# Kernel optimization log

Measured on AMD Instinct MI355X. Metric: run time of the kernel, lower is better.

## Reference

```python
import jax, jax.numpy as jnp
import numpy as np

DIM = 1024
HEADS = 16
DIM_HEAD = 64
DIM_INNER = HEADS * DIM_HEAD
SCALE = DIM_HEAD ** -0.5


def rmsnorm(x, w):
    eps = jnp.asarray(jnp.finfo(x.dtype).eps, x.dtype)
    var = jnp.mean(jnp.square(x), axis=-1, keepdims=True)
    return x * jax.lax.rsqrt(var + eps) * w


def setup_inputs() -> dict:
    key = jax.random.key(0)
    ks = jax.random.split(key, 6)
    tokens = jax.random.normal(ks[0], (2, 2048, DIM), dtype=jnp.float32)
    norm_w = jnp.ones((DIM,), dtype=jnp.float32)
    Wq = jax.random.normal(ks[1], (DIM, DIM_INNER), dtype=jnp.float32) * 0.02
    Wkv = jax.random.normal(ks[2], (DIM, 2 * DIM_INNER), dtype=jnp.float32) * 0.02
    Wout = jax.random.normal(ks[3], (DIM_INNER, DIM), dtype=jnp.float32) * 0.02
    Wg = jax.random.normal(ks[4], (DIM, HEADS), dtype=jnp.float32) * 0.02
    return {"tokens": tokens, "norm_w": norm_w, "Wq": Wq, "Wkv": Wkv, "Wout": Wout, "Wg": Wg}


def reference(tokens, norm_w, Wq, Wkv, Wout, Wg):
    b, n, _ = tokens.shape
    x = rmsnorm(tokens, norm_w)                      # [b, n, dim]
    q = x @ Wq                                       # [b, n, h*d]
    kv = x @ Wkv                                     # self-attention: context = tokens
    k, v = jnp.split(kv, 2, axis=-1)

    def split_heads(t):
        return t.reshape(b, n, HEADS, DIM_HEAD).transpose(0, 2, 1, 3)  # [b, h, n, d]

    q, k, v = map(split_heads, (q, k, v))

    sim = jnp.einsum('bhid,bhjd->bhij', q, k) * SCALE  # [b, h, n, n]
    causal_mask = jnp.triu(jnp.ones((n, n), dtype=bool), k=1)
    sim = jnp.where(causal_mask, jnp.asarray(-jnp.finfo(sim.dtype).max, sim.dtype), sim)
    attn = jax.nn.softmax(sim, axis=-1)
    out = jnp.einsum('bhij,bhjd->bhid', attn, v)       # [b, h, n, d]

    gates = jax.nn.sigmoid(x @ Wg)                     # [b, n, h]
    gates = gates.transpose(0, 2, 1)[..., None]        # [b, h, n, 1]
    out = gates * out

    out = out.transpose(0, 2, 1, 3).reshape(b, n, DIM_INNER)  # merge heads
    return out @ Wout                                  # [b, n, dim]
```

## Files before the change

### kernel.cpp

```cpp
#include <hip/hip_runtime.h>
#include <hip/hip_bf16.h>
#include <math.h>

constexpr int BB = 2;
constexpr int NN = 2048;
constexpr int DM = 1024;
constexpr int NH = 16;
constexpr int HD = 64;
constexpr int DI = NH * HD;
constexpr int MT = BB * NN;
constexpr float SM_SCALE = 0.125f * 1.44269504089f;

typedef __attribute__((ext_vector_type(8))) short short8v;
typedef __attribute__((ext_vector_type(4))) float f32x4;

__device__ inline unsigned cvt_pk_bf16(float lo, float hi) {
  unsigned r;
  asm("v_cvt_pk_bf16_f32 %0, %1, %2" : "=v"(r) : "v"(lo), "v"(hi));
  return r;
}
__device__ inline void pl32_swap(unsigned& a, unsigned& b) {
  asm("v_permlane32_swap_b32 %0, %1" : "+v"(a), "+v"(b));
}
__device__ inline void pl16_swap(unsigned& a, unsigned& b) {
  asm("v_permlane16_swap_b32 %0, %1" : "+v"(a), "+v"(b));
}
__device__ __forceinline__ void gload16(const void* g, void* l) {
  __builtin_amdgcn_global_load_lds(
      (const __attribute__((address_space(1))) unsigned int*)g,
      (__attribute__((address_space(3))) unsigned int*)l, 16, 0, 0);
}

__global__ __launch_bounds__(256) void k_prep(const float* __restrict__ tokens,
                                              const float* __restrict__ norm_w,
                                              const float* __restrict__ Wg,
                                              const float* __restrict__ Wq,
                                              const float* __restrict__ Wkv,
                                              const float* __restrict__ Wout,
                                              __hip_bfloat16* __restrict__ xb,
                                              float* __restrict__ g,
                                              __hip_bfloat16* __restrict__ Wqkvt,
                                              __hip_bfloat16* __restrict__ Woutt) {
  const int bid = blockIdx.x;
  const int t = threadIdx.x;
  if (bid < MT) {
    __shared__ float xs[DM];
    __shared__ float red[4];
    __shared__ float gred[4][16];
    const int tok = bid;
    float4 v = ((const float4*)(tokens + (size_t)tok * DM))[t];
    float ss = v.x * v.x + v.y * v.y + v.z * v.z + v.w * v.w;
#pragma unroll
    for (int m = 1; m < 64; m <<= 1) ss += __shfl_xor(ss, m, 64);
    if ((t & 63) == 0) red[t >> 6] = ss;
    __syncthreads();
    float tot = red[0] + red[1] + red[2] + red[3];
    float inv = rsqrtf(tot * (1.0f / DM) + 1.1920929e-7f);
    float4 wv = ((const float4*)norm_w)[t];
    float4 o;
    o.x = v.x * inv * wv.x;
    o.y = v.y * inv * wv.y;
    o.z = v.z * inv * wv.z;
    o.w = v.w * inv * wv.w;
    uint2 pk = make_uint2(cvt_pk_bf16(o.x, o.y), cvt_pk_bf16(o.z, o.w));
    *(uint2*)(xb + (size_t)tok * DM + t * 4) = pk;
    *(float4*)&xs[t * 4] = o;
    __syncthreads();
    const int h = t & 15, seg = t >> 4, wid = t >> 6;
    const float* xp = &xs[seg * 64];
    const float* wp = Wg + (size_t)(seg * 64) * NH + h;
    float s = 0.f;
#pragma unroll 8
    for (int k = 0; k < 64; k++) s = fmaf(xp[k], wp[(size_t)k * NH], s);
    s += __shfl_xor(s, 16);
    s += __shfl_xor(s, 32);
    if ((t & 63) < 16) gred[wid][h] = s;
    __syncthreads();
    if (t < 16) {
      float tot2 = gred[0][t] + gred[1][t] + gred[2][t] + gred[3][t];
      g[(size_t)tok * NH + t] = 1.f / (1.f + __expf(-tot2));
    }
  } else {
    const int wb = bid - MT;
    const int bx = wb & 127, by = wb >> 7;
    const int kb = by * 32;
    const float* W;
    __hip_bfloat16* dst;
    int N, col0, drow0;
    if (bx < 32) {
      W = Wq; N = DI; col0 = bx * 32; dst = Wqkvt; drow0 = col0;
    } else if (bx < 96) {
      W = Wkv; N = 2 * DI; col0 = (bx - 32) * 32; dst = Wqkvt; drow0 = DI + col0;
    } else {
      W = Wout; N = DM; col0 = (bx - 96) * 32; dst = Woutt; drow0 = col0;
    }
    __shared__ float tile[32][33];
    const int c = t & 31, r8 = t >> 5;
#pragma unroll
    for (int i = 0; i < 4; i++)
      tile[r8 + i * 8][c] = W[(size_t)(kb + r8 + i * 8) * N + col0 + c];
    __syncthreads();
#pragma unroll
    for (int i = 0; i < 4; i++)
      dst[(size_t)(drow0 + r8 + i * 8) * DM + kb + c] = __float2bfloat16(tile[c][r8 + i * 8]);
  }
}

template <int MODE, int BX>
__global__ __launch_bounds__(256) void k_mgemm(const __hip_bfloat16* __restrict__ A,
                                               const __hip_bfloat16* __restrict__ Bt,
                                               float* __restrict__ C,
                                               __hip_bfloat16* __restrict__ OQ,
                                               __hip_bfloat16* __restrict__ OK,
                                               __hip_bfloat16* __restrict__ OV, int Nc) {
  const int nwg = (int)gridDim.x;
  const int cpx = nwg >> 3;
  const int swz = (blockIdx.x & 7) * cpx + (blockIdx.x >> 3);
  const int bxi = swz % BX, byi = swz / BX;

  __shared__ __hip_bfloat16 As[128][32];
  __shared__ __hip_bfloat16 Bs[64][32];
  const int t = threadIdx.x, wid = t >> 6, lane = t & 63;
  const int lq = lane & 15, lg = lane >> 4;
  const int wr = wid >> 1, wc = wid & 1;
  const int m0 = byi * 128, n0 = bxi * 64;
  const int srow = lane >> 2, scol = (lane & 3) * 8;

  const __hip_bfloat16* Ag = A + (size_t)(m0 + wid * 32 + srow) * DM + scol;
  const __hip_bfloat16* Bg = Bt + (size_t)(n0 + wid * 16 + srow) * DM + scol;

  f32x4 acc[4][2];
#pragma unroll
  for (int i = 0; i < 4; i++)
#pragma unroll
    for (int j = 0; j < 2; j++) acc[i][j] = (f32x4){0.f, 0.f, 0.f, 0.f};

  for (int k0 = 0; k0 < DM; k0 += 32) {
    __syncthreads();
    gload16(Ag + k0, &As[wid * 32][0]);
    gload16(Ag + 16 * DM + k0, &As[wid * 32 + 16][0]);
    gload16(Bg + k0, &Bs[wid * 16][0]);
    __syncthreads();
    short8v af[4], bf[2];
#pragma unroll
    for (int i = 0; i < 4; i++) af[i] = *(const short8v*)&As[wr * 64 + i * 16 + lq][lg * 8];
#pragma unroll
    for (int j = 0; j < 2; j++) bf[j] = *(const short8v*)&Bs[wc * 32 + j * 16 + lq][lg * 8];
#pragma unroll
    for (int i = 0; i < 4; i++)
#pragma unroll
      for (int j = 0; j < 2; j++)
        acc[i][j] = __builtin_amdgcn_mfma_f32_16x16x32_bf16(af[i], bf[j], acc[i][j], 0, 0, 0);
  }

#pragma unroll
  for (int i = 0; i < 4; i++) {
    const int mb = m0 + wr * 64 + i * 16 + lg * 4;
#pragma unroll
    for (int j = 0; j < 2; j++) {
      const int c = n0 + wc * 32 + j * 16 + lq;
      if (MODE == 0) {
#pragma unroll
        for (int r = 0; r < 4; r++) C[(size_t)(mb + r) * Nc + c] = acc[i][j][r];
      } else {
        const int b = mb >> 11, nl = mb & (NN - 1);
        if (c < DI) {
          const int h = c >> 6, d = c & 63;
          __hip_bfloat16* dst = OQ + ((size_t)(b * NH + h) * NN + nl) * HD + d;
#pragma unroll
          for (int r = 0; r < 4; r++) dst[(size_t)r * HD] = __float2bfloat16(acc[i][j][r]);
        } else if (c < 2 * DI) {
          const int ck = c - DI;
          const int h = ck >> 6, d = ck & 63;
          __hip_bfloat16* dst = OK + ((size_t)(b * NH + h) * NN + nl) * HD + d;
#pragma unroll
          for (int r = 0; r < 4; r++) dst[(size_t)r * HD] = __float2bfloat16(acc[i][j][r]);
        } else {
          const int cd = c - 2 * DI;
          const int h = cd >> 6, d = cd & 63;
          uint2 pk = make_uint2(cvt_pk_bf16(acc[i][j][0], acc[i][j][1]),
                                cvt_pk_bf16(acc[i][j][2], acc[i][j][3]));
          *(uint2*)(OV + ((size_t)(b * NH + h) * HD + d) * NN + nl) = pk;
        }
      }
    }
  }
}

__global__ __launch_bounds__(64) void k_attn_mfma(const __hip_bfloat16* __restrict__ Qb,
                                                  const __hip_bfloat16* __restrict__ Kb,
                                                  const __hip_bfloat16* __restrict__ Vtb,
                                                  const float* __restrict__ gates,
                                                  __hip_bfloat16* __restrict__ aob,
                                                  float* __restrict__ Opart,
                                                  float* __restrict__ mpart,
                                                  float* __restrict__ lpart) {
  const int bid = blockIdx.x;
  const int xcd = bid & 7;
  const int s = bid >> 3;
  const int gq = s / 96;
  const int t = s % 96;
  const int bh = gq * 8 + xcd;
  const int i = t / 3, j = t % 3;
  int grp, kt0, kt1, chunk;
  if (j < 2) {
    grp = 63 - i;
    chunk = j;
    const int nt = (grp >> 1) + 1;
    const int h0 = (nt + 1) >> 1;
    kt0 = chunk ? h0 : 0;
    kt1 = chunk ? nt : h0;
  } else {
    grp = 31 - i;
    chunk = -1;
    kt0 = 0;
    kt1 = (grp >> 1) + 1;
  }
  const int lane = threadIdx.x;
  const int lg = lane >> 4, lq = lane & 15;
  const int q0 = grp * 32;

  const __hip_bfloat16* Qh = Qb + (size_t)bh * NN * HD;
  const __hip_bfloat16* Kh = Kb + (size_t)bh * NN * HD;
  const __hip_bfloat16* Vh = Vtb + (size_t)bh * HD * NN;

  short8v qf0[2], qf1[2];
#pragma unroll
  for (int ks = 0; ks < 2; ks++) {
    qf0[ks] = *(const short8v*)(Qh + (size_t)(q0 + lq) * HD + ks * 32 + lg * 8);
    qf1[ks] = *(const short8v*)(Qh + (size_t)(q0 + 16 + lq) * HD + ks * 32 + lg * 8);
  }

  f32x4 oacc0[4], oacc1[4];
#pragma unroll
  for (int jx = 0; jx < 4; jx++) {
    oacc0[jx] = (f32x4){0.f, 0.f, 0.f, 0.f};
    oacc1[jx] = (f32x4){0.f, 0.f, 0.f, 0.f};
  }
  float m0r = -3.0e38f, l0p = 0.f, m1r = -3.0e38f, l1p = 0.f;

  auto LOADK = [&](short8v (*kf)[2], int kt) {
    const int kvb = kt * 64;
#pragma unroll
    for (int jx = 0; jx < 4; jx++)
#pragma unroll
      for (int ks = 0; ks < 2; ks++)
        kf[jx][ks] = *(const short8v*)(Kh + (size_t)(kvb + jx * 16 + lq) * HD + ks * 32 + lg * 8);
  };
  auto LOADV = [&](short8v (*vf)[2], int kt) {
    const int kvb = kt * 64;
#pragma unroll
    for (int jx = 0; jx < 4; jx++)
#pragma unroll
      for (int ks = 0; ks < 2; ks++)
        vf[jx][ks] = *(const short8v*)(Vh + (size_t)(jx * 16 + lq) * NN + kvb + ks * 32 + lg * 8);
  };

  auto GROUP = [&](const short8v* qf, f32x4* oacc, float& m_run, float& l_part,
                   int q0g, const short8v (*kf)[2], const short8v (*vf)[2], int kt) {
    const int kvb = kt * 64;
    f32x4 sacc[4];
#pragma unroll
    for (int jx = 0; jx < 4; jx++) sacc[jx] = (f32x4){0.f, 0.f, 0.f, 0.f};
#pragma unroll
    for (int jx = 0; jx < 4; jx++)
#pragma unroll
      for (int ks = 0; ks < 2; ks++)
        sacc[jx] = __builtin_amdgcn_mfma_f32_16x16x32_bf16(kf[jx][ks], qf[ks], sacc[jx], 0, 0, 0);

    const int qg = q0g + lq;
    const bool diag = (kvb + 63 > q0g);
    float ss[4][4];
#pragma unroll
    for (int jx = 0; jx < 4; jx++)
#pragma unroll
      for (int r = 0; r < 4; r++) {
        float v = sacc[jx][r] * SM_SCALE;
        if (diag && (kvb + jx * 16 + lg * 4 + r > qg)) v = -3.0e38f;
        ss[jx][r] = v;
      }

    float tmax = -3.0e38f;
#pragma unroll
    for (int jx = 0; jx < 4; jx++)
#pragma unroll
      for (int r = 0; r < 4; r++) tmax = fmaxf(tmax, ss[jx][r]);

    if (!__all(tmax <= m_run + 8.0f)) {
      float tr = fmaxf(tmax, __shfl_xor(tmax, 16));
      tr = fmaxf(tr, __shfl_xor(tr, 32));
      const float mnew = fmaxf(m_run, tr);
      const float cf = exp2f(m_run - mnew);
      l_part *= cf;
#pragma unroll
      for (int jx = 0; jx < 4; jx++)
#pragma unroll
        for (int r = 0; r < 4; r++) oacc[jx][r] *= cf;
      m_run = mnew;
    }

    float psum = 0.f;
    unsigned upk[4], vpk[4];
#pragma unroll
    for (int jx = 0; jx < 4; jx++) {
      float p0 = exp2f(ss[jx][0] - m_run), p1 = exp2f(ss[jx][1] - m_run);
      float p2 = exp2f(ss[jx][2] - m_run), p3 = exp2f(ss[jx][3] - m_run);
      psum += (p0 + p1) + (p2 + p3);
      upk[jx] = cvt_pk_bf16(p0, p1);
      vpk[jx] = cvt_pk_bf16(p2, p3);
    }
    l_part += psum;

#pragma unroll
    for (int ks = 0; ks < 2; ks++) {
      unsigned w0 = upk[2 * ks], w2 = upk[2 * ks + 1];
      unsigned w1 = vpk[2 * ks], w3 = vpk[2 * ks + 1];
      pl32_swap(w0, w2);
      pl16_swap(w0, w2);
      pl32_swap(w1, w3);
      pl16_swap(w1, w3);
      int4 bw = make_int4((int)w0, (int)w1, (int)w2, (int)w3);
      short8v pb = __builtin_bit_cast(short8v, bw);
#pragma unroll
      for (int jx = 0; jx < 4; jx++)
        oacc[jx] = __builtin_amdgcn_mfma_f32_16x16x32_bf16(vf[jx][ks], pb, oacc[jx], 0, 0, 0);
    }
  };

  short8v kfA[4][2], kfB[4][2], vf[4][2];
  LOADK(kfA, kt0);
  int kt = kt0;
  while (true) {
    LOADV(vf, kt);
    if (kt + 1 < kt1) LOADK(kfB, kt + 1);
    GROUP(qf0, oacc0, m0r, l0p, q0, kfA, vf, kt);
    GROUP(qf1, oacc1, m1r, l1p, q0 + 16, kfA, vf, kt);
    if (++kt == kt1) break;
    LOADV(vf, kt);
    if (kt + 1 < kt1) LOADK(kfA, kt + 1);
    GROUP(qf0, oacc0, m0r, l0p, q0, kfB, vf, kt);
    GROUP(qf1, oacc1, m1r, l1p, q0 + 16, kfB, vf, kt);
    if (++kt == kt1) break;
  }

  float l0 = l0p + __shfl_xor(l0p, 16);
  l0 += __shfl_xor(l0, 32);
  float l1 = l1p + __shfl_xor(l1p, 16);
  l1 += __shfl_xor(l1, 32);

  if (chunk >= 0) {
    const int gi = grp - 32;
    const size_t pidx = (size_t)(bh * 32 + gi) * 2 + chunk;
    float* Op = Opart + pidx * 2048;
#pragma unroll
    for (int jx = 0; jx < 4; jx++) {
      *(f32x4*)(Op + lq * 64 + jx * 16 + lg * 4) = oacc0[jx];
      *(f32x4*)(Op + (16 + lq) * 64 + jx * 16 + lg * 4) = oacc1[jx];
    }
    if (lane < 16) {
      mpart[pidx * 32 + lane] = m0r;
      mpart[pidx * 32 + 16 + lane] = m1r;
      lpart[pidx * 32 + lane] = l0;
      lpart[pidx * 32 + 16 + lane] = l1;
    }
    return;
  }

  const int b = bh >> 4, h = bh & 15;
  const float g0 = gates[((size_t)(b * NN + q0 + lq)) * NH + h];
  const float g1 = gates[((size_t)(b * NN + q0 + 16 + lq)) * NH + h];
  const float sc0 = g0 / l0, sc1 = g1 / l1;
  __shared__ float ots[32][68];
#pragma unroll
  for (int jx = 0; jx < 4; jx++)
#pragma unroll
    for (int r = 0; r < 4; r++) {
      ots[lq][jx * 16 + lg * 4 + r] = oacc0[jx][r] * sc0;
      ots[16 + lq][jx * 16 + lg * 4 + r] = oacc1[jx][r] * sc1;
    }
  __syncthreads();
  const int d0 = (lane & 3) * 16;
#pragma unroll
  for (int rr = 0; rr < 2; rr++) {
    const int rl = rr * 16 + (lane >> 2);
    __hip_bfloat16* aor = aob + ((size_t)(b * NN + q0 + rl)) * DI + h * HD + d0;
#pragma unroll
    for (int u = 0; u < 4; u++) {
      uint2 pk = make_uint2(
          cvt_pk_bf16(ots[rl][d0 + 4 * u + 0], ots[rl][d0 + 4 * u + 1]),
          cvt_pk_bf16(ots[rl][d0 + 4 * u + 2], ots[rl][d0 + 4 * u + 3]));
      *(uint2*)(aor + 4 * u) = pk;
    }
  }
}

__global__ __launch_bounds__(256) void k_attn_combine(const float* __restrict__ Opart,
                                                      const float* __restrict__ mpart,
                                                      const float* __restrict__ lpart,
                                                      const float* __restrict__ gates,
                                                      __hip_bfloat16* __restrict__ aob) {
  const int hg = blockIdx.x;
  const int h = hg >> 5, gi = hg & 31;
  const int grp = 32 + gi;
  const int t = threadIdx.x;
  const int row = t >> 3, dq = (t & 7) * 8;
  const size_t p0 = (size_t)hg * 2, p1 = p0 + 1;
  const float m0 = mpart[p0 * 32 + row], m1 = mpart[p1 * 32 + row];
  const float l0 = lpart[p0 * 32 + row], l1 = lpart[p1 * 32 + row];
  const float M = fmaxf(m0, m1);
  const float a0 = exp2f(m0 - M), a1 = exp2f(m1 - M);
  const float L = a0 * l0 + a1 * l1;
  const int b = h >> 4, hh = h & 15;
  const int grow = grp * 32 + row;
  const float sc = gates[((size_t)(b * NN + grow)) * NH + hh] / L;
  const float* O0 = Opart + p0 * 2048 + row * 64 + dq;
  const float* O1 = Opart + p1 * 2048 + row * 64 + dq;
  unsigned pk[4];
#pragma unroll
  for (int u = 0; u < 4; u++) {
    float x0 = (a0 * O0[2 * u + 0] + a1 * O1[2 * u + 0]) * sc;
    float x1 = (a0 * O0[2 * u + 1] + a1 * O1[2 * u + 1]) * sc;
    pk[u] = cvt_pk_bf16(x0, x1);
  }
  __hip_bfloat16* dst = aob + ((size_t)(b * NN + grow)) * DI + hh * 64 + dq;
  *(uint4*)dst = make_uint4(pk[0], pk[1], pk[2], pk[3]);
}

extern "C" void kernel_launch(void* const* d_in, const int* in_sizes, int n_in,
                              void* d_out, int out_size, void* d_ws, size_t ws_size,
                              hipStream_t stream) {
  const float* tokens = (const float*)d_in[0];
  const float* norm_w = (const float*)d_in[1];
  const float* Wq     = (const float*)d_in[2];
  const float* Wkv    = (const float*)d_in[3];
  const float* Wout   = (const float*)d_in[4];
  const float* Wg     = (const float*)d_in[5];
  float* out = (float*)d_out;

  float* ws = (float*)d_ws;
  float* gb = ws;
  __hip_bfloat16* xb    = (__hip_bfloat16*)(gb + (size_t)MT * NH);
  __hip_bfloat16* aob   = xb + (size_t)MT * DM;
  __hip_bfloat16* Qb    = aob + (size_t)MT * DM;
  __hip_bfloat16* Kb    = Qb + (size_t)MT * DI;
  __hip_bfloat16* Vtb   = Kb + (size_t)MT * DI;
  __hip_bfloat16* Wqkvt = Vtb + (size_t)MT * DI;
  __hip_bfloat16* Woutt = Wqkvt + (size_t)3 * DI * DM;
  float* Opart = (float*)(Woutt + (size_t)DM * DI);
  float* mpart = Opart + (size_t)2048 * 2048;
  float* lpart = mpart + (size_t)2048 * 32;

  k_prep<<<dim3(MT + 4096), 256, 0, stream>>>(tokens, norm_w, Wg, Wq, Wkv, Wout,
                                              xb, gb, Wqkvt, Woutt);
  k_mgemm<3, 48><<<dim3(48 * 32), 256, 0, stream>>>(
      xb, Wqkvt, nullptr, Qb, Kb, Vtb, 3 * DI);
  k_attn_mfma<<<dim3(32 * 96), 64, 0, stream>>>(Qb, Kb, Vtb, gb, aob, Opart, mpart, lpart);
  k_attn_combine<<<dim3(1024), 256, 0, stream>>>(Opart, mpart, lpart, gb, aob);
  k_mgemm<0, 16><<<dim3(16 * 32), 256, 0, stream>>>(
      aob, Woutt, out, nullptr, nullptr, nullptr, DM);
}
```

Baseline: 166.4 us.

## Fuse split-KV combine into attention kernel via atomic last-arriver counter

Removes the separate combine kernel launch by having the second of the two split-KV workgroups for each (head, row-group) merge the partial outputs, using a per-tile atomic counter with threadfences. Counters are zeroed in the prep kernel. This saves one launch and its dependency gap, but the final merge now runs on a single 64-lane wave with strided scalar loads instead of a 256-thread block.

```diff
diff --git a/kernel.cpp b/kernel.cpp
--- a/kernel.cpp
+++ b/kernel.cpp
@@ -40,9 +40,11 @@
                                               __hip_bfloat16* __restrict__ xb,
                                               float* __restrict__ g,
                                               __hip_bfloat16* __restrict__ Wqkvt,
-                                              __hip_bfloat16* __restrict__ Woutt) {
+                                              __hip_bfloat16* __restrict__ Woutt,
+                                              int* __restrict__ cnt) {
   const int bid = blockIdx.x;
   const int t = threadIdx.x;
+  if (bid < 4) cnt[bid * 256 + t] = 0;
   if (bid < MT) {
     __shared__ float xs[DM];
     __shared__ float red[4];
@@ -194,7 +196,8 @@
                                                   __hip_bfloat16* __restrict__ aob,
                                                   float* __restrict__ Opart,
                                                   float* __restrict__ mpart,
-                                                  float* __restrict__ lpart) {
+                                                  float* __restrict__ lpart,
+                                                  int* __restrict__ cnt) {
   const int bid = blockIdx.x;
   const int xcd = bid & 7;
   const int s = bid >> 3;
@@ -348,9 +351,12 @@
   float l1 = l1p + __shfl_xor(l1p, 16);
   l1 += __shfl_xor(l1, 32);
 
+  const int b = bh >> 4, h = bh & 15;
+
   if (chunk >= 0) {
     const int gi = grp - 32;
-    const size_t pidx = (size_t)(bh * 32 + gi) * 2 + chunk;
+    const int hg = bh * 32 + gi;
+    const size_t pidx = (size_t)hg * 2 + chunk;
     float* Op = Opart + pidx * 2048;
 #pragma unroll
     for (int jx = 0; jx < 4; jx++) {
@@ -363,10 +369,39 @@
       lpart[pidx * 32 + lane] = l0;
       lpart[pidx * 32 + 16 + lane] = l1;
     }
+    __threadfence();
+    int old = 0;
+    if (lane == 0) old = atomicAdd(&cnt[hg], 1);
+    old = __shfl(old, 0, 64);
+    if (old == 1) {
+      __threadfence();
+      const size_t pA = (size_t)hg * 2, pB = pA + 1;
+      const int row = lane >> 1, dq0 = (lane & 1) * 32;
+      const float mA = mpart[pA * 32 + row], mB = mpart[pB * 32 + row];
+      const float lA = lpart[pA * 32 + row], lB = lpart[pB * 32 + row];
+      const float M = fmaxf(mA, mB);
+      const float a0 = exp2f(mA - M), a1 = exp2f(mB - M);
+      const float L = a0 * lA + a1 * lB;
+      const int grow = grp * 32 + row;
+      const float sc = gates[((size_t)(b * NN + grow)) * NH + h] / L;
+      const float* OA = Opart + pA * 2048 + row * 64 + dq0;
+      const float* OB = Opart + pB * 2048 + row * 64 + dq0;
+      __hip_bfloat16* dst = aob + ((size_t)(b * NN + grow)) * DI + h * HD + dq0;
+#pragma unroll
+      for (int u = 0; u < 4; u++) {
+        unsigned pk[4];
+#pragma unroll
+        for (int w = 0; w < 4; w++) {
+          const int e = u * 8 + 2 * w;
+          pk[w] = cvt_pk_bf16((a0 * OA[e] + a1 * OB[e]) * sc,
+                              (a0 * OA[e + 1] + a1 * OB[e + 1]) * sc);
+        }
+        *(uint4*)(dst + u * 8) = make_uint4(pk[0], pk[1], pk[2], pk[3]);
+      }
+    }
     return;
   }
 
-  const int b = bh >> 4, h = bh & 15;
   const float g0 = gates[((size_t)(b * NN + q0 + lq)) * NH + h];
   const float g1 = gates[((size_t)(b * NN + q0 + 16 + lq)) * NH + h];
   const float sc0 = g0 / l0, sc1 = g1 / l1;
@@ -392,38 +427,6 @@
       *(uint2*)(aor + 4 * u) = pk;
     }
   }
-}
-
-__global__ __launch_bounds__(256) void k_attn_combine(const float* __restrict__ Opart,
-                                                      const float* __restrict__ mpart,
-                                                      const float* __restrict__ lpart,
-                                                      const float* __restrict__ gates,
-                                                      __hip_bfloat16* __restrict__ aob) {
-  const int hg = blockIdx.x;
-  const int h = hg >> 5, gi = hg & 31;
-  const int grp = 32 + gi;
-  const int t = threadIdx.x;
-  const int row = t >> 3, dq = (t & 7) * 8;
-  const size_t p0 = (size_t)hg * 2, p1 = p0 + 1;
-  const float m0 = mpart[p0 * 32 + row], m1 = mpart[p1 * 32 + row];
-  const float l0 = lpart[p0 * 32 + row], l1 = lpart[p1 * 32 + row];
-  const float M = fmaxf(m0, m1);
-  const float a0 = exp2f(m0 - M), a1 = exp2f(m1 - M);
-  const float L = a0 * l0 + a1 * l1;
-  const int b = h >> 4, hh = h & 15;
-  const int grow = grp * 32 + row;
-  const float sc = gates[((size_t)(b * NN + grow)) * NH + hh] / L;
-  const float* O0 = Opart + p0 * 2048 + row * 64 + dq;
-  const float* O1 = Opart + p1 * 2048 + row * 64 + dq;
-  unsigned pk[4];
-#pragma unroll
-  for (int u = 0; u < 4; u++) {
-    float x0 = (a0 * O0[2 * u + 0] + a1 * O1[2 * u + 0]) * sc;
-    float x1 = (a0 * O0[2 * u + 1] + a1 * O1[2 * u + 1]) * sc;
-    pk[u] = cvt_pk_bf16(x0, x1);
-  }
-  __hip_bfloat16* dst = aob + ((size_t)(b * NN + grow)) * DI + hh * 64 + dq;
-  *(uint4*)dst = make_uint4(pk[0], pk[1], pk[2], pk[3]);
 }
 
 extern "C" void kernel_launch(void* const* d_in, const int* in_sizes, int n_in,
@@ -449,13 +452,14 @@
   float* Opart = (float*)(Woutt + (size_t)DM * DI);
   float* mpart = Opart + (size_t)2048 * 2048;
   float* lpart = mpart + (size_t)2048 * 32;
+  int*   cnt   = (int*)(lpart + (size_t)2048 * 32);
 
   k_prep<<<dim3(MT + 4096), 256, 0, stream>>>(tokens, norm_w, Wg, Wq, Wkv, Wout,
-                                              xb, gb, Wqkvt, Woutt);
+                                              xb, gb, Wqkvt, Woutt, cnt);
   k_mgemm<3, 48><<<dim3(48 * 32), 256, 0, stream>>>(
       xb, Wqkvt, nullptr, Qb, Kb, Vtb, 3 * DI);
-  k_attn_mfma<<<dim3(32 * 96), 64, 0, stream>>>(Qb, Kb, Vtb, gb, aob, Opart, mpart, lpart);
-  k_attn_combine<<<dim3(1024), 256, 0, stream>>>(Opart, mpart, lpart, gb, aob);
+  k_attn_mfma<<<dim3(32 * 96), 64, 0, stream>>>(Qb, Kb, Vtb, gb, aob,
+                                                Opart, mpart, lpart, cnt);
   k_mgemm<0, 16><<<dim3(16 * 32), 256, 0, stream>>>(
       aob, Woutt, out, nullptr, nullptr, nullptr, DM);
 }
```

Measured after the change: 245.6 us. +47.5%, slower.
